# Kernel optimization log

Hardware: AMD Instinct MI355X
Metric: run time of the kernel (lower is better)

## Reference

```python
import jax, jax.numpy as jnp
import numpy as np

HEAD_DIM = 128
L2_EPS = 1e-6


def l2norm(x):
    # RMS-style L2Norm: computed in fp32, cast back (matches L2Norm.forward)
    x32 = x.astype(jnp.float32)
    y = x32 * jax.lax.rsqrt(jnp.mean(x32 * x32, axis=-1, keepdims=True) + L2_EPS)
    return y.astype(x.dtype)


def setup_inputs() -> dict:
    key = jax.random.key(0)
    ks = jax.random.split(key, 8)
    B, S, D = 16, 1, 4096
    NKV, HD, MAXS = 8, HEAD_DIM, 4096
    w_scale = 0.02
    return {
        "x": jax.random.normal(ks[0], (B, S, D), dtype=jnp.float32),
        "wq": jax.random.normal(ks[1], (D, D), dtype=jnp.float32) * w_scale,
        "wk": jax.random.normal(ks[2], (D, NKV * HD), dtype=jnp.float32) * w_scale,
        "wv": jax.random.normal(ks[3], (D, NKV * HD), dtype=jnp.float32) * w_scale,
        "wo": jax.random.normal(ks[4], (D, D), dtype=jnp.float32) * w_scale,
        "cache_k": jax.random.normal(ks[5], (B, MAXS, NKV, HD), dtype=jnp.float32),
        "cache_v": jax.random.normal(ks[6], (B, MAXS, NKV, HD), dtype=jnp.float32),
        "freqs_complex": jax.random.normal(ks[7], (1, 64), dtype=jnp.float32),  # unused, as in source
        "start_pos": 4095,
    }


def reference(x, wq, wk, wv, wo, cache_k, cache_v, freqs_complex, start_pos):
    b, s, d = x.shape
    hd = HEAD_DIM
    n_kv = cache_k.shape[2]
    n_q = wq.shape[1] // hd
    n_rep = n_q // n_kv

    # QKV projections (Linear, no bias)
    xq = (x @ wq).reshape(b, s, n_q, hd)
    xk = (x @ wk).reshape(b, s, n_kv, hd)
    xv = (x @ wv).reshape(b, s, n_kv, hd)

    # qk_norm active since dim <= 4096
    xq = l2norm(xq)
    xk = l2norm(xk)

    # KV-cache append at start_pos (start_pos is a static Python int)
    cache_k = jax.lax.dynamic_update_slice(cache_k, xk, (0, start_pos, 0, 0))
    cache_v = jax.lax.dynamic_update_slice(cache_v, xv, (0, start_pos, 0, 0))
    keys = cache_k[:, : start_pos + s]    # [b, T, n_kv, hd]
    values = cache_v[:, : start_pos + s]  # [b, T, n_kv, hd]

    # GQA: group query heads as (n_kv, n_rep); equivalent to repeat_kv without
    # materializing the repeated KV tensors.
    xq = xq.reshape(b, s, n_kv, n_rep, hd)
    scores = jnp.einsum("bqgrd,bkgd->bgrqk", xq, keys) / np.float32(np.sqrt(hd))
    scores = jax.nn.softmax(scores.astype(jnp.float32), axis=-1).astype(xq.dtype)
    out = jnp.einsum("bgrqk,bkgd->bqgrd", scores, values).reshape(b, s, n_q * hd)
    return out @ wo
```

## Files before the change

### kernel.cpp

```cpp
#include <hip/hip_runtime.h>

#define D_MODEL 4096
#define NKV     8
#define NREP    4
#define HD      128
#define BATCH   16
#define SEQ     4096
#define NCOLS   6144
#define SPLITS  32
#define KC      128
#define NS      16
#define CHUNK   256

#define OFF_QKVP 0
#define OFF_ATTO 0
#define OFF_WOP  0
#define OFF_QKV  3145728
#define OFF_ATTM 3244032
#define OFF_ATTL 3252224
#define OFF_XO   3260416

__global__ __launch_bounds__(256) void qkv_partial(
    const float* __restrict__ x, const float* __restrict__ wq,
    const float* __restrict__ wk, const float* __restrict__ wv,
    float* __restrict__ part)
{
  int tid = threadIdx.x;
  int col = blockIdx.x * 256 + tid;
  int sp  = blockIdx.y;
  const float* w; int c; int N;
  if (col < 4096)      { w = wq; c = col;        N = 4096; }
  else if (col < 5120) { w = wk; c = col - 4096; N = 1024; }
  else                 { w = wv; c = col - 5120; N = 1024; }
  int k0 = sp * KC;
  const float* wp = w + (size_t)k0 * N + c;
  float acc[BATCH];
#pragma unroll
  for (int b = 0; b < BATCH; ++b) acc[b] = 0.f;
#pragma unroll 2
  for (int kk = 0; kk < KC; kk += 8) {
    float wr[8];
#pragma unroll
    for (int j = 0; j < 8; ++j) wr[j] = wp[(size_t)j * N];
#pragma unroll
    for (int b = 0; b < BATCH; ++b) {
      float4 xa = *reinterpret_cast<const float4*>(x + b * D_MODEL + k0 + kk);
      float4 xb = *reinterpret_cast<const float4*>(x + b * D_MODEL + k0 + kk + 4);
      float t = acc[b];
      t = fmaf(xa.x, wr[0], t); t = fmaf(xa.y, wr[1], t);
      t = fmaf(xa.z, wr[2], t); t = fmaf(xa.w, wr[3], t);
      t = fmaf(xb.x, wr[4], t); t = fmaf(xb.y, wr[5], t);
      t = fmaf(xb.z, wr[6], t); t = fmaf(xb.w, wr[7], t);
      acc[b] = t;
    }
    wp += (size_t)8 * N;
  }
#pragma unroll
  for (int b = 0; b < BATCH; ++b)
    part[(size_t)(sp * BATCH + b) * NCOLS + col] = acc[b];
}

__global__ __launch_bounds__(128) void qkv_finalize(
    const float* __restrict__ part, float* __restrict__ qkv)
{
  __shared__ float red[2];
  int blk = blockIdx.x;
  int b = blk / 48, h = blk - b * 48;
  int col = h * HD + threadIdx.x;
  float v = 0.f;
#pragma unroll
  for (int s = 0; s < SPLITS; ++s)
    v += part[(size_t)(s * BATCH + b) * NCOLS + col];
  float ss = v * v;
#pragma unroll
  for (int off = 32; off; off >>= 1) ss += __shfl_xor(ss, off);
  if ((threadIdx.x & 63) == 0) red[threadIdx.x >> 6] = ss;
  __syncthreads();
  float tot = red[0] + red[1];
  if (h < 40)
    v *= rsqrtf(tot * (1.f / 128.f) + 1e-6f);
  qkv[(size_t)b * NCOLS + col] = v;
}

__global__ __launch_bounds__(256, 4) void attn_partial(
    const float* __restrict__ cache_k, const float* __restrict__ cache_v,
    const float* __restrict__ qkv,
    float* __restrict__ attO, float* __restrict__ attM, float* __restrict__ attL)
{
  __shared__ float qs[NREP * HD];
  __shared__ float sc[NREP * CHUNK];
  int tid = threadIdx.x;
  int bg = blockIdx.x;
  int sp = blockIdx.y;
  int b = bg >> 3, g = bg & 7;

  const float* qsrc = qkv + (size_t)b * NCOLS + g * (NREP * HD);
  for (int i = tid; i < NREP * HD; i += 256) qs[i] = qsrc[i];
  __syncthreads();

  int pos0 = sp * CHUNK;

  {
    int pos = pos0 + tid;
    const float* kv = (pos == SEQ - 1)
        ? (qkv + (size_t)b * NCOLS + 4096 + g * HD)
        : (cache_k + ((size_t)b * SEQ * NKV + g) * HD + (size_t)pos * (NKV * HD));
    float a[NREP];
#pragma unroll
    for (int r = 0; r < NREP; ++r) a[r] = 0.f;
#pragma unroll
    for (int c = 0; c < 4; ++c) {
      float4 kr[8];
#pragma unroll
      for (int j = 0; j < 8; ++j)
        kr[j] = *reinterpret_cast<const float4*>(kv + c * 32 + j * 4);
#pragma unroll
      for (int r = 0; r < NREP; ++r) {
        float s = 0.f;
#pragma unroll
        for (int j = 0; j < 8; ++j) {
          float4 qv = *reinterpret_cast<const float4*>(qs + r * HD + c * 32 + j * 4);
          s += kr[j].x * qv.x + kr[j].y * qv.y + kr[j].z * qv.z + kr[j].w * qv.w;
        }
        a[r] += s;
      }
    }
    const float scl = 0.08838834764831845f;
#pragma unroll
    for (int r = 0; r < NREP; ++r) sc[r * CHUNK + tid] = a[r] * scl;
  }
  __syncthreads();

  int wv_ = tid >> 6, lane = tid & 63;
  float m_reg, l_reg;
  {
    float vals[4];
    float m = -1e30f;
#pragma unroll
    for (int i = 0; i < 4; ++i) { vals[i] = sc[wv_ * CHUNK + i * 64 + lane]; m = fmaxf(m, vals[i]); }
#pragma unroll
    for (int off = 32; off; off >>= 1) m = fmaxf(m, __shfl_xor(m, off));
    float l = 0.f;
#pragma unroll
    for (int i = 0; i < 4; ++i) { float p = __expf(vals[i] - m); sc[wv_ * CHUNK + i * 64 + lane] = p; l += p; }
#pragma unroll
    for (int off = 32; off; off >>= 1) l += __shfl_xor(l, off);
    m_reg = m; l_reg = l;
  }
  __syncthreads();

  {
    int dl = lane * 2;
    const float* vbase  = cache_v + ((size_t)b * SEQ * NKV + g) * HD;
    const float* vfresh = qkv + (size_t)b * NCOLS + 5120 + g * HD;
    const float* pr = sc + wv_ * CHUNK;
    float ax = 0.f, ay = 0.f;
    for (int j = 0; j < CHUNK; j += 8) {
#pragma unroll
      for (int u = 0; u < 8; ++u) {
        int pos = pos0 + j + u;
        const float* vp = (pos == SEQ - 1) ? vfresh : (vbase + (size_t)pos * (NKV * HD));
        float2 vd = *reinterpret_cast<const float2*>(vp + dl);
        float p = pr[j + u];
        ax = fmaf(p, vd.x, ax);
        ay = fmaf(p, vd.y, ay);
      }
    }
    size_t base = (size_t)(bg * NS + sp);
    *reinterpret_cast<float2*>(attO + base * (NREP * HD) + wv_ * HD + dl) = make_float2(ax, ay);
    if (lane == 0) { attM[base * 4 + wv_] = m_reg; attL[base * 4 + wv_] = l_reg; }
  }
}

__global__ __launch_bounds__(512) void attn_combine(
    const float* __restrict__ attO, const float* __restrict__ attM,
    const float* __restrict__ attL, float* __restrict__ xo)
{
  int bg = blockIdx.x;
  int tid = threadIdx.x;
  int r = tid >> 7;
  float m_s[NS];
  float M = -1e30f;
#pragma unroll
  for (int s = 0; s < NS; ++s) {
    m_s[s] = attM[(size_t)(bg * NS + s) * 4 + r];
    M = fmaxf(M, m_s[s]);
  }
  float L = 0.f, o = 0.f;
#pragma unroll
  for (int s = 0; s < NS; ++s) {
    float f = __expf(m_s[s] - M);
    L += attL[(size_t)(bg * NS + s) * 4 + r] * f;
    o += attO[(size_t)(bg * NS + s) * 512 + tid] * f;
  }
  int b = bg >> 3, g = bg & 7;
  xo[(size_t)b * D_MODEL + g * 512 + tid] = o / L;
}

__global__ __launch_bounds__(256) void wo_partial(
    const float* __restrict__ xo, const float* __restrict__ wo,
    float* __restrict__ part)
{
  int tid = threadIdx.x;
  int col = blockIdx.x * 256 + tid;
  int sp  = blockIdx.y;
  int k0 = sp * KC;
  const float* wp = wo + (size_t)k0 * D_MODEL + col;
  float acc[BATCH];
#pragma unroll
  for (int b = 0; b < BATCH; ++b) acc[b] = 0.f;
#pragma unroll 2
  for (int kk = 0; kk < KC; kk += 8) {
    float wr[8];
#pragma unroll
    for (int j = 0; j < 8; ++j) wr[j] = wp[(size_t)j * D_MODEL];
#pragma unroll
    for (int b = 0; b < BATCH; ++b) {
      float4 xa = *reinterpret_cast<const float4*>(xo + b * D_MODEL + k0 + kk);
      float4 xb = *reinterpret_cast<const float4*>(xo + b * D_MODEL + k0 + kk + 4);
      float t = acc[b];
      t = fmaf(xa.x, wr[0], t); t = fmaf(xa.y, wr[1], t);
      t = fmaf(xa.z, wr[2], t); t = fmaf(xa.w, wr[3], t);
      t = fmaf(xb.x, wr[4], t); t = fmaf(xb.y, wr[5], t);
      t = fmaf(xb.z, wr[6], t); t = fmaf(xb.w, wr[7], t);
      acc[b] = t;
    }
    wp += (size_t)8 * D_MODEL;
  }
#pragma unroll
  for (int b = 0; b < BATCH; ++b)
    part[(size_t)(sp * BATCH + b) * D_MODEL + col] = acc[b];
}

__global__ __launch_bounds__(256) void wo_finalize(
    const float* __restrict__ part, float* __restrict__ out)
{
  int i = blockIdx.x * 256 + threadIdx.x;
  float v = 0.f;
#pragma unroll
  for (int s = 0; s < SPLITS; ++s)
    v += part[(size_t)s * (BATCH * D_MODEL) + i];
  out[i] = v;
}

extern "C" void kernel_launch(void* const* d_in, const int* in_sizes, int n_in,
                              void* d_out, int out_size, void* d_ws, size_t ws_size,
                              hipStream_t stream) {
  const float* x       = (const float*)d_in[0];
  const float* wq      = (const float*)d_in[1];
  const float* wk      = (const float*)d_in[2];
  const float* wv      = (const float*)d_in[3];
  const float* wo      = (const float*)d_in[4];
  const float* cache_k = (const float*)d_in[5];
  const float* cache_v = (const float*)d_in[6];
  float* out  = (float*)d_out;
  float* wsf  = (float*)d_ws;
  float* qkvp = wsf + OFF_QKVP;
  float* qkv  = wsf + OFF_QKV;
  float* attO = wsf + OFF_ATTO;
  float* attM = wsf + OFF_ATTM;
  float* attL = wsf + OFF_ATTL;
  float* xo   = wsf + OFF_XO;
  float* wop  = wsf + OFF_WOP;

  qkv_partial <<<dim3(24, 32), 256, 0, stream>>>(x, wq, wk, wv, qkvp);
  qkv_finalize<<<BATCH * 48, 128, 0, stream>>>(qkvp, qkv);
  attn_partial<<<dim3(BATCH * NKV, NS), 256, 0, stream>>>(cache_k, cache_v, qkv, attO, attM, attL);
  attn_combine<<<BATCH * NKV, 512, 0, stream>>>(attO, attM, attL, xo);
  wo_partial  <<<dim3(16, 32), 256, 0, stream>>>(xo, wo, wop);
  wo_finalize <<<256, 256, 0, stream>>>(wop, out);
}
```

Baseline: 740.5 us.

## Stage activations in LDS, widen weight loads, and coalesce attention K/V access

```diff
diff --git a/kernel.cpp b/kernel.cpp
--- a/kernel.cpp
+++ b/kernel.cpp
@@ -25,39 +25,53 @@
     const float* __restrict__ wk, const float* __restrict__ wv,
     float* __restrict__ part)
 {
+  __shared__ float xs[BATCH * KC];
   int tid = threadIdx.x;
-  int col = blockIdx.x * 256 + tid;
   int sp  = blockIdx.y;
-  const float* w; int c; int N;
-  if (col < 4096)      { w = wq; c = col;        N = 4096; }
-  else if (col < 5120) { w = wk; c = col - 4096; N = 1024; }
-  else                 { w = wv; c = col - 5120; N = 1024; }
-  int k0 = sp * KC;
-  const float* wp = w + (size_t)k0 * N + c;
-  float acc[BATCH];
-#pragma unroll
-  for (int b = 0; b < BATCH; ++b) acc[b] = 0.f;
+  int k0  = sp * KC;
+  for (int i = tid; i < BATCH * KC; i += 256) {
+    int b = i >> 7, kk = i & (KC - 1);
+    xs[i] = x[(size_t)b * D_MODEL + k0 + kk];
+  }
+  __syncthreads();
+
+  int w = tid >> 6, lane = tid & 63;
+  int col = blockIdx.x * 512 + w * 128 + lane * 2;
+  const float* wm; int c; int N;
+  if (col < 4096)      { wm = wq; c = col;        N = 4096; }
+  else if (col < 5120) { wm = wk; c = col - 4096; N = 1024; }
+  else                 { wm = wv; c = col - 5120; N = 1024; }
+  const float* wp = wm + (size_t)k0 * N + c;
+
+  float accx[BATCH], accy[BATCH];
+#pragma unroll
+  for (int b = 0; b < BATCH; ++b) { accx[b] = 0.f; accy[b] = 0.f; }
 #pragma unroll 2
   for (int kk = 0; kk < KC; kk += 8) {
-    float wr[8];
-#pragma unroll
-    for (int j = 0; j < 8; ++j) wr[j] = wp[(size_t)j * N];
+    float2 wr[8];
+#pragma unroll
+    for (int j = 0; j < 8; ++j)
+      wr[j] = *reinterpret_cast<const float2*>(wp + (size_t)(kk + j) * N);
 #pragma unroll
     for (int b = 0; b < BATCH; ++b) {
-      float4 xa = *reinterpret_cast<const float4*>(x + b * D_MODEL + k0 + kk);
-      float4 xb = *reinterpret_cast<const float4*>(x + b * D_MODEL + k0 + kk + 4);
-      float t = acc[b];
-      t = fmaf(xa.x, wr[0], t); t = fmaf(xa.y, wr[1], t);
-      t = fmaf(xa.z, wr[2], t); t = fmaf(xa.w, wr[3], t);
-      t = fmaf(xb.x, wr[4], t); t = fmaf(xb.y, wr[5], t);
-      t = fmaf(xb.z, wr[6], t); t = fmaf(xb.w, wr[7], t);
-      acc[b] = t;
+      float4 xa = *reinterpret_cast<const float4*>(xs + b * KC + kk);
+      float4 xb = *reinterpret_cast<const float4*>(xs + b * KC + kk + 4);
+      float tx = accx[b], ty = accy[b];
+      tx = fmaf(xa.x, wr[0].x, tx); ty = fmaf(xa.x, wr[0].y, ty);
+      tx = fmaf(xa.y, wr[1].x, tx); ty = fmaf(xa.y, wr[1].y, ty);
+      tx = fmaf(xa.z, wr[2].x, tx); ty = fmaf(xa.z, wr[2].y, ty);
+      tx = fmaf(xa.w, wr[3].x, tx); ty = fmaf(xa.w, wr[3].y, ty);
+      tx = fmaf(xb.x, wr[4].x, tx); ty = fmaf(xb.x, wr[4].y, ty);
+      tx = fmaf(xb.y, wr[5].x, tx); ty = fmaf(xb.y, wr[5].y, ty);
+      tx = fmaf(xb.z, wr[6].x, tx); ty = fmaf(xb.z, wr[6].y, ty);
+      tx = fmaf(xb.w, wr[7].x, tx); ty = fmaf(xb.w, wr[7].y, ty);
+      accx[b] = tx; accy[b] = ty;
     }
-    wp += (size_t)8 * N;
   }
 #pragma unroll
   for (int b = 0; b < BATCH; ++b)
-    part[(size_t)(sp * BATCH + b) * NCOLS + col] = acc[b];
+    *reinterpret_cast<float2*>(&part[(size_t)(sp * BATCH + b) * NCOLS + col]) =
+        make_float2(accx[b], accy[b]);
 }
 
 __global__ __launch_bounds__(128) void qkv_finalize(
@@ -89,6 +103,7 @@
 {
   __shared__ float qs[NREP * HD];
   __shared__ float sc[NREP * CHUNK];
+  __shared__ float op[4 * NREP * HD];
   int tid = threadIdx.x;
   int bg = blockIdx.x;
   int sp = blockIdx.y;
@@ -99,35 +114,41 @@
   __syncthreads();
 
   int pos0 = sp * CHUNK;
+  const float* kbase  = cache_k + ((size_t)b * SEQ * NKV + g) * HD;
+  const float* kfresh = qkv + (size_t)b * NCOLS + 4096 + g * HD;
+  const float scl = 0.08838834764831845f;
 
   {
-    int pos = pos0 + tid;
-    const float* kv = (pos == SEQ - 1)
-        ? (qkv + (size_t)b * NCOLS + 4096 + g * HD)
-        : (cache_k + ((size_t)b * SEQ * NKV + g) * HD + (size_t)pos * (NKV * HD));
-    float a[NREP];
-#pragma unroll
-    for (int r = 0; r < NREP; ++r) a[r] = 0.f;
-#pragma unroll
-    for (int c = 0; c < 4; ++c) {
+    int pl = tid >> 2, dq = tid & 3;
+#pragma unroll 2
+    for (int pass = 0; pass < 4; ++pass) {
+      int pc  = pass * 64 + pl;
+      int pos = pos0 + pc;
+      const float* kv = (pos == SEQ - 1) ? kfresh
+                                         : (kbase + (size_t)pos * (NKV * HD));
       float4 kr[8];
 #pragma unroll
       for (int j = 0; j < 8; ++j)
-        kr[j] = *reinterpret_cast<const float4*>(kv + c * 32 + j * 4);
+        kr[j] = *reinterpret_cast<const float4*>(kv + j * 16 + dq * 4);
+      float a[NREP];
+#pragma unroll
+      for (int r = 0; r < NREP; ++r) a[r] = 0.f;
+#pragma unroll
+      for (int j = 0; j < 8; ++j) {
+#pragma unroll
+        for (int r = 0; r < NREP; ++r) {
+          float4 qv = *reinterpret_cast<const float4*>(qs + r * HD + j * 16 + dq * 4);
+          a[r] += kr[j].x * qv.x + kr[j].y * qv.y + kr[j].z * qv.z + kr[j].w * qv.w;
+        }
+      }
 #pragma unroll
       for (int r = 0; r < NREP; ++r) {
-        float s = 0.f;
-#pragma unroll
-        for (int j = 0; j < 8; ++j) {
-          float4 qv = *reinterpret_cast<const float4*>(qs + r * HD + c * 32 + j * 4);
-          s += kr[j].x * qv.x + kr[j].y * qv.y + kr[j].z * qv.z + kr[j].w * qv.w;
-        }
-        a[r] += s;
+        a[r] += __shfl_xor(a[r], 1);
+        a[r] += __shfl_xor(a[r], 2);
       }
+      float out = (dq == 0) ? a[0] : (dq == 1) ? a[1] : (dq == 2) ? a[2] : a[3];
+      sc[dq * CHUNK + pc] = out * scl;
     }
-    const float scl = 0.08838834764831845f;
-#pragma unroll
-    for (int r = 0; r < NREP; ++r) sc[r * CHUNK + tid] = a[r] * scl;
   }
   __syncthreads();
 
@@ -150,26 +171,44 @@
   __syncthreads();
 
   {
+    int quarter = wv_;
     int dl = lane * 2;
     const float* vbase  = cache_v + ((size_t)b * SEQ * NKV + g) * HD;
     const float* vfresh = qkv + (size_t)b * NCOLS + 5120 + g * HD;
-    const float* pr = sc + wv_ * CHUNK;
-    float ax = 0.f, ay = 0.f;
-    for (int j = 0; j < CHUNK; j += 8) {
+    float a00=0,a01=0,a10=0,a11=0,a20=0,a21=0,a30=0,a31=0;
+    int pb = pos0 + quarter * 64;
+    for (int j = 0; j < 64; j += 8) {
 #pragma unroll
       for (int u = 0; u < 8; ++u) {
-        int pos = pos0 + j + u;
+        int pos = pb + j + u;
         const float* vp = (pos == SEQ - 1) ? vfresh : (vbase + (size_t)pos * (NKV * HD));
         float2 vd = *reinterpret_cast<const float2*>(vp + dl);
-        float p = pr[j + u];
-        ax = fmaf(p, vd.x, ax);
-        ay = fmaf(p, vd.y, ay);
+        int qp = quarter * 64 + j + u;
+        float p0 = sc[0 * CHUNK + qp];
+        float p1 = sc[1 * CHUNK + qp];
+        float p2 = sc[2 * CHUNK + qp];
+        float p3 = sc[3 * CHUNK + qp];
+        a00 = fmaf(p0, vd.x, a00); a01 = fmaf(p0, vd.y, a01);
+        a10 = fmaf(p1, vd.x, a10); a11 = fmaf(p1, vd.y, a11);
+        a20 = fmaf(p2, vd.x, a20); a21 = fmaf(p2, vd.y, a21);
+        a30 = fmaf(p3, vd.x, a30); a31 = fmaf(p3, vd.y, a31);
       }
     }
-    size_t base = (size_t)(bg * NS + sp);
-    *reinterpret_cast<float2*>(attO + base * (NREP * HD) + wv_ * HD + dl) = make_float2(ax, ay);
-    if (lane == 0) { attM[base * 4 + wv_] = m_reg; attL[base * 4 + wv_] = l_reg; }
-  }
+    *reinterpret_cast<float2*>(op + (quarter * NREP + 0) * HD + dl) = make_float2(a00, a01);
+    *reinterpret_cast<float2*>(op + (quarter * NREP + 1) * HD + dl) = make_float2(a10, a11);
+    *reinterpret_cast<float2*>(op + (quarter * NREP + 2) * HD + dl) = make_float2(a20, a21);
+    *reinterpret_cast<float2*>(op + (quarter * NREP + 3) * HD + dl) = make_float2(a30, a31);
+  }
+  __syncthreads();
+
+  size_t base = (size_t)(bg * NS + sp);
+  for (int i = tid; i < NREP * HD; i += 256) {
+    int r = i >> 7, d = i & 127;
+    float o = op[(0*NREP + r)*HD + d] + op[(1*NREP + r)*HD + d]
+            + op[(2*NREP + r)*HD + d] + op[(3*NREP + r)*HD + d];
+    attO[base * (NREP * HD) + i] = o;
+  }
+  if (lane == 0) { attM[base * 4 + wv_] = m_reg; attL[base * 4 + wv_] = l_reg; }
 }
 
 __global__ __launch_bounds__(512) void attn_combine(
@@ -201,35 +240,49 @@
     const float* __restrict__ xo, const float* __restrict__ wo,
     float* __restrict__ part)
 {
+  __shared__ float xs[BATCH * KC];
   int tid = threadIdx.x;
-  int col = blockIdx.x * 256 + tid;
   int sp  = blockIdx.y;
-  int k0 = sp * KC;
+  int k0  = sp * KC;
+  for (int i = tid; i < BATCH * KC; i += 256) {
+    int b = i >> 7, kk = i & (KC - 1);
+    xs[i] = xo[(size_t)b * D_MODEL + k0 + kk];
+  }
+  __syncthreads();
+
+  int w = tid >> 6, lane = tid & 63;
+  int col = blockIdx.x * 512 + w * 128 + lane * 2;
   const float* wp = wo + (size_t)k0 * D_MODEL + col;
-  float acc[BATCH];
-#pragma unroll
-  for (int b = 0; b < BATCH; ++b) acc[b] = 0.f;
+
+  float accx[BATCH], accy[BATCH];
+#pragma unroll
+  for (int b = 0; b < BATCH; ++b) { accx[b] = 0.f; accy[b] = 0.f; }
 #pragma unroll 2
   for (int kk = 0; kk < KC; kk += 8) {
-    float wr[8];
-#pragma unroll
-    for (int j = 0; j < 8; ++j) wr[j] = wp[(size_t)j * D_MODEL];
+    float2 wr[8];
+#pragma unroll
+    for (int j = 0; j < 8; ++j)
+      wr[j] = *reinterpret_cast<const float2*>(wp + (size_t)(kk + j) * D_MODEL);
 #pragma unroll
     for (int b = 0; b < BATCH; ++b) {
-      float4 xa = *reinterpret_cast<const float4*>(xo + b * D_MODEL + k0 + kk);
-      float4 xb = *reinterpret_cast<const float4*>(xo + b * D_MODEL + k0 + kk + 4);
-      float t = acc[b];
-      t = fmaf(xa.x, wr[0], t); t = fmaf(xa.y, wr[1], t);
-      t = fmaf(xa.z, wr[2], t); t = fmaf(xa.w, wr[3], t);
-      t = fmaf(xb.x, wr[4], t); t = fmaf(xb.y, wr[5], t);
-      t = fmaf(xb.z, wr[6], t); t = fmaf(xb.w, wr[7], t);
-      acc[b] = t;
+      float4 xa = *reinterpret_cast<const float4*>(xs + b * KC + kk);
+      float4 xb = *reinterpret_cast<const float4*>(xs + b * KC + kk + 4);
+      float tx = accx[b], ty = accy[b];
+      tx = fmaf(xa.x, wr[0].x, tx); ty = fmaf(xa.x, wr[0].y, ty);
+      tx = fmaf(xa.y, wr[1].x, tx); ty = fmaf(xa.y, wr[1].y, ty);
+      tx = fmaf(xa.z, wr[2].x, tx); ty = fmaf(xa.z, wr[2].y, ty);
+      tx = fmaf(xa.w, wr[3].x, tx); ty = fmaf(xa.w, wr[3].y, ty);
+      tx = fmaf(xb.x, wr[4].x, tx); ty = fmaf(xb.x, wr[4].y, ty);
+      tx = fmaf(xb.y, wr[5].x, tx); ty = fmaf(xb.y, wr[5].y, ty);
+      tx = fmaf(xb.z, wr[6].x, tx); ty = fmaf(xb.z, wr[6].y, ty);
+      tx = fmaf(xb.w, wr[7].x, tx); ty = fmaf(xb.w, wr[7].y, ty);
+      accx[b] = tx; accy[b] = ty;
     }
-    wp += (size_t)8 * D_MODEL;
   }
 #pragma unroll
   for (int b = 0; b < BATCH; ++b)
-    part[(size_t)(sp * BATCH + b) * D_MODEL + col] = acc[b];
+    *reinterpret_cast<float2*>(&part[(size_t)(sp * BATCH + b) * D_MODEL + col]) =
+        make_float2(accx[b], accy[b]);
 }
 
 __global__ __launch_bounds__(256) void wo_finalize(
@@ -263,10 +316,10 @@
   float* xo   = wsf + OFF_XO;
   float* wop  = wsf + OFF_WOP;
 
-  qkv_partial <<<dim3(24, 32), 256, 0, stream>>>(x, wq, wk, wv, qkvp);
+  qkv_partial <<<dim3(12, 32), 256, 0, stream>>>(x, wq, wk, wv, qkvp);
   qkv_finalize<<<BATCH * 48, 128, 0, stream>>>(qkvp, qkv);
   attn_partial<<<dim3(BATCH * NKV, NS), 256, 0, stream>>>(cache_k, cache_v, qkv, attO, attM, attL);
   attn_combine<<<BATCH * NKV, 512, 0, stream>>>(attO, attM, attL, xo);
-  wo_partial  <<<dim3(16, 32), 256, 0, stream>>>(xo, wo, wop);
+  wo_partial  <<<dim3(8, 32), 256, 0, stream>>>(xo, wo, wop);
   wo_finalize <<<256, 256, 0, stream>>>(wop, out);
 }
```

After: 691.1 us. -6.7%, faster.
